# Performance work log

Hardware: AMD Instinct MI355X
Metric: run time of the kernel (lower is better)

## Reference

```python
import jax, jax.numpy as jnp
import numpy as np

NEG = -1000000000.0

def setup_inputs() -> dict:
    key = jax.random.key(0)
    ks = jax.random.split(key, 6)
    B, V, F, H = 8, 4, 256, 768
    video_features = jax.random.normal(ks[0], (B, V, F, H), dtype=jnp.float32)
    video_attention_mask = jax.random.randint(ks[1], (B, V, F), 0, 2) > 0  # True = masked
    s = 1.0 / np.sqrt(H)
    Wqkv = jax.random.normal(ks[2], (3 * H, H), dtype=jnp.float32) * s
    bqkv = jax.random.normal(ks[3], (3 * H,), dtype=jnp.float32) * 0.01
    Wo = jax.random.normal(ks[4], (H, H), dtype=jnp.float32) * s
    bo = jax.random.normal(ks[5], (H,), dtype=jnp.float32) * 0.01
    return {"video_features": video_features, "video_attention_mask": video_attention_mask,
            "Wqkv": Wqkv, "bqkv": bqkv, "Wo": Wo, "bo": bo}

def reference(video_features, video_attention_mask, Wqkv, bqkv, Wo, bo):
    B, V, F, H = video_features.shape
    n_heads = 12
    head_dim = H // n_heads
    S = V * F  # total frames
    x = video_features.reshape(B, S, H)
    mask = video_attention_mask.reshape(B, S)
    # fused QKV projection (torch Linear: x @ W.T + b)
    qkv = x @ Wqkv.T + bqkv                      # [B, S, 3H]
    qkv = qkv.reshape(B, S, n_heads, 3 * head_dim).transpose(0, 2, 1, 3)  # [B, h, S, 3d]
    q, k, v = jnp.split(qkv, 3, axis=-1)         # each [B, h, S, d]
    scores = jnp.einsum('bhqd,bhkd->bhqk', q, k) / np.sqrt(head_dim)
    scores = jnp.where(mask[:, None, None, :], NEG, scores)
    attn = jax.nn.softmax(scores, axis=-1)       # dropout p=0 (eval) -> identity
    out = jnp.einsum('bhqk,bhkd->bhqd', attn, v) # [B, h, S, d]
    out = out.transpose(0, 2, 1, 3).reshape(B, S, H)
    out = out @ Wo.T + bo
    return out.reshape(B, V, F, H)
```

## Files before the change

### kernel.cpp

```cpp
#include <hip/hip_runtime.h>
#include <stdint.h>

typedef unsigned short u16;
typedef unsigned int u32;
typedef __attribute__((ext_vector_type(8))) unsigned short u16x8;
typedef __attribute__((ext_vector_type(4))) unsigned short u16x4;
typedef __attribute__((ext_vector_type(4))) float f32x4;
typedef __attribute__((ext_vector_type(16))) float f32x16;
typedef __attribute__((ext_vector_type(4))) float floatx4;
typedef __attribute__((ext_vector_type(8))) __bf16 bf16x8;


__device__ __forceinline__ u16 f2bf(float f) {
  union { float f; unsigned u; } c; c.f = f;
  unsigned r = c.u + 0x7fffu + ((c.u >> 16) & 1u);
  return (u16)(r >> 16);
}

__device__ __forceinline__ u32 packbf2(float lo, float hi) {
  return (u32)f2bf(lo) | ((u32)f2bf(hi) << 16);
}

__device__ __forceinline__ bf16x8 ld_bf8(const u16* p) {
  return __builtin_bit_cast(bf16x8, *(const u16x8*)p);
}

__device__ __forceinline__ float fexp2(float x) {
#if __has_builtin(__builtin_amdgcn_exp2f)
  return __builtin_amdgcn_exp2f(x);
#else
  float r; asm("v_exp_f32 %0, %1" : "=v"(r) : "v"(x)); return r;
#endif
}

__device__ __forceinline__ void glds16(const void* g, void* l) {
  __builtin_amdgcn_global_load_lds(
      (const __attribute__((address_space(1))) void*)g,
      (__attribute__((address_space(3))) void*)l, 16, 0, 0);
}

__global__ void convert_kernel(const float* __restrict__ x,
                               const float* __restrict__ w1,
                               const float* __restrict__ w2,
                               u16* __restrict__ xb,
                               u16* __restrict__ w1b,
                               u16* __restrict__ w2b) {
  const long NX = 6291456 / 4, NW1 = 1769472 / 4, NW2 = 589824 / 4;
  const long total = NX + NW1 + NW2;
  for (long i = (long)blockIdx.x * 256 + threadIdx.x; i < total;
       i += (long)gridDim.x * 256) {
    const float* src; u16* dst; long j;
    if (i < NX)            { src = x;  dst = xb;  j = i; }
    else if (i < NX + NW1) { src = w1; dst = w1b; j = i - NX; }
    else                   { src = w2; dst = w2b; j = i - NX - NW1; }
    floatx4 v = ((const floatx4*)src)[j];
    u16x4 o;
    o[0] = f2bf(v[0]); o[1] = f2bf(v[1]); o[2] = f2bf(v[2]); o[3] = f2bf(v[3]);
    ((u16x4*)dst)[j] = o;
  }
}

__global__ __launch_bounds__(256, 2)
void qkv_gemm(const u16* __restrict__ A, const u16* __restrict__ W,
              const float* __restrict__ bias,
              u16* __restrict__ qb, u16* __restrict__ kb, u16* __restrict__ vtb) {
  __shared__ __align__(16) u16 lA[2][128 * 64];
  __shared__ __align__(16) u16 lB[2][128 * 64];
  const int tid = threadIdx.x;
  const int lane = tid & 63, wid = tid >> 6;
  const int wm = wid >> 1, wn = wid & 1;
  const int l15 = lane & 15, l4 = lane >> 4;
  const int h7 = l15 & 7;

  const int p = blockIdx.x;
  const int xcd = p & 7, i = p >> 3;
  const int by = xcd * 8 + i / 18;
  const int bx = i % 18;
  const int rowA0 = by * 128, rowB0 = bx * 128;

  const int rlo = lane >> 3;
  const int swz = (lane & 7) ^ rlo;
  const u16* ga = A + (size_t)(rowA0 + wid * 8 + rlo) * 768 + swz * 8;
  const u16* gb = W + (size_t)(rowB0 + wid * 8 + rlo) * 768 + swz * 8;

  f32x4 acc[4][4];
  const f32x4 vz = {0.f, 0.f, 0.f, 0.f};
#pragma unroll
  for (int ii = 0; ii < 4; ++ii)
#pragma unroll
    for (int j = 0; j < 4; ++j) acc[ii][j] = vz;

#define QSTAGE(buf, k0)                                          \
  {                                                              \
    _Pragma("unroll") for (int j = 0; j < 4; ++j) {              \
      glds16(ga + (k0) + j * 32 * 768, lA[buf] + j * 2048 + wid * 512); \
      glds16(gb + (k0) + j * 32 * 768, lB[buf] + j * 2048 + wid * 512); \
    }                                                            \
  }

  QSTAGE(0, 0);

  for (int ks = 0; ks < 12; ++ks) {
    const int cur = ks & 1;
    __builtin_amdgcn_s_barrier();
    if (ks < 11) {
      QSTAGE(cur ^ 1, (ks + 1) * 64);
      asm volatile("s_waitcnt vmcnt(8)" ::: "memory");
    } else {
      asm volatile("s_waitcnt vmcnt(0)" ::: "memory");
    }
    __builtin_amdgcn_s_barrier();
    __builtin_amdgcn_sched_barrier(0);

    bf16x8 af[4][2], bfr[4][2];
#pragma unroll
    for (int mi = 0; mi < 4; ++mi)
#pragma unroll
      for (int kk = 0; kk < 2; ++kk)
        af[mi][kk] = ld_bf8(lA[cur] + (wm * 64 + mi * 16 + l15) * 64 +
                            (((kk * 4 + l4) ^ h7) * 8));
#pragma unroll
    for (int ni = 0; ni < 4; ++ni)
#pragma unroll
      for (int kk = 0; kk < 2; ++kk)
        bfr[ni][kk] = ld_bf8(lB[cur] + (wn * 64 + ni * 16 + l15) * 64 +
                             (((kk * 4 + l4) ^ h7) * 8));
    __builtin_amdgcn_s_setprio(1);
#pragma unroll
    for (int mi = 0; mi < 4; ++mi)
#pragma unroll
      for (int ni = 0; ni < 4; ++ni)
#pragma unroll
        for (int kk = 0; kk < 2; ++kk)
          acc[mi][ni] = __builtin_amdgcn_mfma_f32_16x16x32_bf16(
              af[mi][kk], bfr[ni][kk], acc[mi][ni], 0, 0, 0);
    __builtin_amdgcn_s_setprio(0);
  }
#undef QSTAGE

  const float QSC = 0.125f * 1.44269504088896f;
#pragma unroll
  for (int ni = 0; ni < 4; ++ni) {
    int n = rowB0 + wn * 64 + ni * 16 + l15;
    int h = n / 192;
    int r3 = n - h * 192;
    int t = r3 >> 6, dd = r3 & 63;
    float bn_ = bias[n];
#pragma unroll
    for (int mi = 0; mi < 4; ++mi) {
#pragma unroll
      for (int r = 0; r < 4; ++r) {
        int m = rowA0 + wm * 64 + mi * 16 + l4 * 4 + r;
        int b = m >> 10, s = m & 1023;
        size_t bh = (size_t)(b * 12 + h);
        float v = acc[mi][ni][r] + bn_;
        if (t == 0)
          qb[bh * 65536 + (size_t)s * 64 + dd] = f2bf(v * QSC);
        else if (t == 1)
          kb[bh * 65536 + (size_t)s * 64 + dd] = f2bf(v);
        else
          vtb[bh * 65536 + (size_t)dd * 1024 + s] = f2bf(v);
      }
    }
  }
}

__global__ __launch_bounds__(256, 3)
void attn_kernel(const u16* __restrict__ qb, const u16* __restrict__ kb,
                 const u16* __restrict__ vtb, const void* __restrict__ maskp,
                 u16* __restrict__ x2) {
  const int bh = blockIdx.x, qt = blockIdx.y;
  const int b = bh / 12, h = bh - b * 12;
  const int tid = threadIdx.x;
  const int w = tid >> 6, lane = tid & 63;
  const int l31 = lane & 31, hi = lane >> 5;

  __shared__ float mbias[1024];
  __shared__ int any_big;
  __shared__ __align__(16) u16 plds[4][32][40];
  __shared__ __align__(16) u16 kvs[16384];

  if (tid == 0) any_big = 0;
  __syncthreads();
  {
    const unsigned* mu = (const unsigned*)maskp;
    int loc = 0;
    for (int i = tid; i < 2048; i += 256)
      if (mu[i] > 1u) loc = 1;
    if (loc) atomicOr(&any_big, 1);
  }
  __syncthreads();
  const float CEXP = 23.0831206542234f;
  if (any_big) {
    const unsigned char* mb = (const unsigned char*)maskp;
    for (int i = tid; i < 1024; i += 256)
      mbias[i] = mb[b * 1024 + i] ? -100000.0f : -CEXP;
  } else {
    const int* mi_ = (const int*)maskp;
    for (int i = tid; i < 1024; i += 256)
      mbias[i] = mi_[b * 1024 + i] ? -100000.0f : -CEXP;
  }

  const size_t base = (size_t)bh * 65536;
  const int q0w = qt * 128 + w * 32;

  const int rlo = lane >> 3;
  const int cg = (lane & 7) ^ (rlo & 7);
  const int srow = w * 8 + rlo;
  const u16* kg0 = kb + base + (size_t)srow * 64 + cg * 8;
  const u16* vg0 = vtb + base + (size_t)srow * 1024 + cg * 8;
  u16* kd0 = kvs + w * 512;
  u16* vd0 = kvs + 4096 + w * 512;

  bf16x8 qf[4];
#pragma unroll
  for (int dstep = 0; dstep < 4; ++dstep)
    qf[dstep] = ld_bf8(qb + base + (size_t)(q0w + l31) * 64 + dstep * 16 + hi * 8);

  f32x16 o[2];
#pragma unroll
  for (int dh = 0; dh < 2; ++dh)
#pragma unroll
    for (int r = 0; r < 16; ++r) o[dh][r] = 0.f;
  float ps = 0.f;

  glds16(kg0, kd0);
  glds16(kg0 + 32 * 64, kd0 + 2048);
  glds16(vg0, vd0);
  glds16(vg0 + 32 * 1024, vd0 + 2048);
  __syncthreads();

  for (int kt = 0; kt < 16; ++kt) {
    const int cur = kt & 1;
    if (kt < 15) {
      const int nxt = cur ^ 1;
      glds16(kg0 + (kt + 1) * 4096, kd0 + nxt * 8192);
      glds16(kg0 + (kt + 1) * 4096 + 32 * 64, kd0 + nxt * 8192 + 2048);
      glds16(vg0 + (kt + 1) * 64, vd0 + nxt * 8192);
      glds16(vg0 + (kt + 1) * 64 + 32 * 1024, vd0 + nxt * 8192 + 2048);
    }

    const u16* Kl = kvs + cur * 8192;
    const u16* Vl = kvs + cur * 8192 + 4096;

#pragma unroll
    for (int kk = 0; kk < 2; ++kk) {
      f32x16 s;
#pragma unroll
      for (int r = 0; r < 16; ++r) s[r] = 0.f;
      const int rk = kk * 32 + l31;
      __builtin_amdgcn_s_setprio(1);
#pragma unroll
      for (int dstep = 0; dstep < 4; ++dstep) {
        bf16x8 kf = ld_bf8(Kl + rk * 64 + ((dstep * 2 + hi) ^ (rk & 7)) * 8);
        s = __builtin_amdgcn_mfma_f32_32x32x16_bf16(kf, qf[dstep], s, 0, 0, 0);
      }
      __builtin_amdgcn_s_setprio(0);
#pragma unroll
      for (int g = 0; g < 4; ++g) {
        f32x4 bv = *(const f32x4*)(mbias + kt * 64 + kk * 32 + g * 8 + hi * 4);
        float p0 = fexp2(s[g * 4 + 0] + bv[0]);
        float p1 = fexp2(s[g * 4 + 1] + bv[1]);
        float p2 = fexp2(s[g * 4 + 2] + bv[2]);
        float p3 = fexp2(s[g * 4 + 3] + bv[3]);
        ps += (p0 + p1) + (p2 + p3);
        const int colb = g * 8 + hi * 4;
        *(u32*)&plds[w][l31][colb]     = packbf2(p0, p1);
        *(u32*)&plds[w][l31][colb + 2] = packbf2(p2, p3);
      }

      __builtin_amdgcn_s_setprio(1);
#pragma unroll
      for (int t = 0; t < 2; ++t) {
        bf16x8 pf = ld_bf8(&plds[w][l31][t * 16 + hi * 8]);
#pragma unroll
        for (int dh = 0; dh < 2; ++dh) {
          const int rv = dh * 32 + l31;
          const int gv = kk * 4 + t * 2 + hi;
          bf16x8 vf = ld_bf8(Vl + rv * 64 + (gv ^ (rv & 7)) * 8);
          o[dh] = __builtin_amdgcn_mfma_f32_32x32x16_bf16(vf, pf, o[dh], 0, 0, 0);
        }
      }
      __builtin_amdgcn_s_setprio(0);
    }

    __syncthreads();
  }

  ps += __shfl_xor(ps, 32, 64);
  float inv = 1.0f / ps;

  u16* obuf = kvs + w * 2304;
#pragma unroll
  for (int dh = 0; dh < 2; ++dh)
#pragma unroll
    for (int j = 0; j < 8; ++j) {
      u32 v = packbf2(o[dh][2 * j] * inv, o[dh][2 * j + 1] * inv);
      int col = dh * 32 + 8 * (j >> 1) + 4 * hi + 2 * (j & 1);
      *(u32*)(obuf + l31 * 72 + col) = v;
    }

  {
    int row2 = lane >> 1, ch = lane & 1;
    const u16* srcp = obuf + row2 * 72 + ch * 32;
    u16x8 t0 = *(const u16x8*)(srcp);
    u16x8 t1 = *(const u16x8*)(srcp + 8);
    u16x8 t2 = *(const u16x8*)(srcp + 16);
    u16x8 t3 = *(const u16x8*)(srcp + 24);
    size_t m = (size_t)b * 1024 + qt * 128 + w * 32 + row2;
    u16* dst = x2 + m * 768 + h * 64 + ch * 32;
    *(u16x8*)dst = t0;
    *(u16x8*)(dst + 8) = t1;
    *(u16x8*)(dst + 16) = t2;
    *(u16x8*)(dst + 24) = t3;
  }
}

__global__ __launch_bounds__(256, 2)
void out_gemm(const u16* __restrict__ A, const u16* __restrict__ W,
              const float* __restrict__ bias, float* __restrict__ out) {
  __shared__ __align__(16) u16 lA[2][128 * 64];
  __shared__ __align__(16) u16 lB[2][128 * 64];
  const int tid = threadIdx.x;
  const int lane = tid & 63, wid = tid >> 6;
  const int wm = wid >> 1, wn = wid & 1;
  const int l15 = lane & 15, l4 = lane >> 4;
  const int h7 = l15 & 7;

  const int p = blockIdx.x;
  const int xcd = p & 7, i = p >> 3;
  const int by = xcd * 8 + i / 6;
  const int bx = i % 6;
  const int rowA0 = by * 128, rowB0 = bx * 128;

  const int rlo = lane >> 3;
  const int swz = (lane & 7) ^ rlo;
  const u16* ga = A + (size_t)(rowA0 + wid * 8 + rlo) * 768 + swz * 8;
  const u16* gb = W + (size_t)(rowB0 + wid * 8 + rlo) * 768 + swz * 8;

  f32x4 acc[4][4];
  const f32x4 vz = {0.f, 0.f, 0.f, 0.f};
#pragma unroll
  for (int ii = 0; ii < 4; ++ii)
#pragma unroll
    for (int j = 0; j < 4; ++j) acc[ii][j] = vz;

#define OSTAGE(buf, k0)                                          \
  {                                                              \
    _Pragma("unroll") for (int j = 0; j < 4; ++j) {              \
      glds16(ga + (k0) + j * 32 * 768, lA[buf] + j * 2048 + wid * 512); \
      glds16(gb + (k0) + j * 32 * 768, lB[buf] + j * 2048 + wid * 512); \
    }                                                            \
  }

  OSTAGE(0, 0);

  for (int ks = 0; ks < 12; ++ks) {
    const int cur = ks & 1;
    __builtin_amdgcn_s_barrier();
    if (ks < 11) {
      OSTAGE(cur ^ 1, (ks + 1) * 64);
      asm volatile("s_waitcnt vmcnt(8)" ::: "memory");
    } else {
      asm volatile("s_waitcnt vmcnt(0)" ::: "memory");
    }
    __builtin_amdgcn_s_barrier();
    __builtin_amdgcn_sched_barrier(0);

    bf16x8 af[4][2], bfr[4][2];
#pragma unroll
    for (int mi = 0; mi < 4; ++mi)
#pragma unroll
      for (int kk = 0; kk < 2; ++kk)
        af[mi][kk] = ld_bf8(lA[cur] + (wm * 64 + mi * 16 + l15) * 64 +
                            (((kk * 4 + l4) ^ h7) * 8));
#pragma unroll
    for (int ni = 0; ni < 4; ++ni)
#pragma unroll
      for (int kk = 0; kk < 2; ++kk)
        bfr[ni][kk] = ld_bf8(lB[cur] + (wn * 64 + ni * 16 + l15) * 64 +
                             (((kk * 4 + l4) ^ h7) * 8));
    __builtin_amdgcn_s_setprio(1);
#pragma unroll
    for (int mi = 0; mi < 4; ++mi)
#pragma unroll
      for (int ni = 0; ni < 4; ++ni)
#pragma unroll
        for (int kk = 0; kk < 2; ++kk)
          acc[mi][ni] = __builtin_amdgcn_mfma_f32_16x16x32_bf16(
              af[mi][kk], bfr[ni][kk], acc[mi][ni], 0, 0, 0);
    __builtin_amdgcn_s_setprio(0);
  }
#undef OSTAGE

#pragma unroll
  for (int ni = 0; ni < 4; ++ni) {
    int n = rowB0 + wn * 64 + ni * 16 + l15;
    float bn_ = bias[n];
#pragma unroll
    for (int mi = 0; mi < 4; ++mi)
#pragma unroll
      for (int r = 0; r < 4; ++r) {
        int m = rowA0 + wm * 64 + mi * 16 + l4 * 4 + r;
        out[(size_t)m * 768 + n] = acc[mi][ni][r] + bn_;
      }
  }
}

extern "C" void kernel_launch(void* const* d_in, const int* in_sizes, int n_in,
                              void* d_out, int out_size, void* d_ws, size_t ws_size,
                              hipStream_t stream) {
  const float* x    = (const float*)d_in[0];
  const void*  mask = d_in[1];
  const float* wqkv = (const float*)d_in[2];
  const float* bqkv = (const float*)d_in[3];
  const float* wo   = (const float*)d_in[4];
  const float* bo   = (const float*)d_in[5];
  float* out = (float*)d_out;

  u16* ws = (u16*)d_ws;
  u16* xbf   = ws;
  u16* wqkvb = ws + 6291456;
  u16* wob   = ws + 8060928;
  u16* qbuf  = ws + 8650752;
  u16* kbuf  = ws + 14942208;
  u16* vtbuf = ws + 21233664;
  u16* x2buf = ws + 27525120;

  convert_kernel<<<2048, 256, 0, stream>>>(x, wqkv, wo, xbf, wqkvb, wob);
  qkv_gemm<<<1152, 256, 0, stream>>>(xbf, wqkvb, bqkv, qbuf, kbuf, vtbuf);
  attn_kernel<<<dim3(96, 8), 256, 0, stream>>>(qbuf, kbuf, vtbuf, mask, x2buf);
  out_gemm<<<384, 256, 0, stream>>>(x2buf, wob, bo, out);
}
```

Before: 127.0 us.

## Retile QKV GEMM to 128x192 head-aligned tiles with LDS-staged coalesced epilogue

The QKV projection GEMM now uses 128x192 output tiles, so each tile covers exactly one head's q/k/v columns. It runs a three-stage LDS pipeline with a K step of 32 and a new swizzled layout that packs two rows per 64-element LDS line. The epilogue stages q, k and transposed v through LDS and writes them with 16-byte coalesced stores, replacing the scattered 2-byte global stores (worst for the transposed V). The cost is more accumulator registers per thread (24 f32x4) and more barriers per K step, which could lower occupancy.

```diff
diff --git a/kernel.cpp b/kernel.cpp
--- a/kernel.cpp
+++ b/kernel.cpp
@@ -64,104 +64,158 @@
 void qkv_gemm(const u16* __restrict__ A, const u16* __restrict__ W,
               const float* __restrict__ bias,
               u16* __restrict__ qb, u16* __restrict__ kb, u16* __restrict__ vtb) {
-  __shared__ __align__(16) u16 lA[2][128 * 64];
-  __shared__ __align__(16) u16 lB[2][128 * 64];
+  __shared__ __align__(16) u16 lds[30720];
   const int tid = threadIdx.x;
   const int lane = tid & 63, wid = tid >> 6;
   const int wm = wid >> 1, wn = wid & 1;
   const int l15 = lane & 15, l4 = lane >> 4;
-  const int h7 = l15 & 7;
 
   const int p = blockIdx.x;
   const int xcd = p & 7, i = p >> 3;
-  const int by = xcd * 8 + i / 18;
-  const int bx = i % 18;
-  const int rowA0 = by * 128, rowB0 = bx * 128;
+  const int by = xcd * 8 + i / 12;
+  const int bx = i % 12;
+  const int rowA0 = by * 128, rowB0 = bx * 192;
 
   const int rlo = lane >> 3;
-  const int swz = (lane & 7) ^ rlo;
-  const u16* ga = A + (size_t)(rowA0 + wid * 8 + rlo) * 768 + swz * 8;
-  const u16* gb = W + (size_t)(rowB0 + wid * 8 + rlo) * 768 + swz * 8;
-
-  f32x4 acc[4][4];
+  const u16* gA[2];
+  const u16* gB[3];
+#pragma unroll
+  for (int c = 0; c < 2; ++c) {
+    int mr = wid * 16 + c * 8 + rlo;
+    int sl = (lane & 7) ^ (mr & 7);
+    gA[c] = A + (size_t)(rowA0 + 2 * mr + (sl >> 2)) * 768 + (sl & 3) * 8;
+  }
+#pragma unroll
+  for (int c = 0; c < 3; ++c) {
+    int mr = wid * 24 + c * 8 + rlo;
+    int sl = (lane & 7) ^ (mr & 7);
+    gB[c] = W + (size_t)(rowB0 + 2 * mr + (sl >> 2)) * 768 + (sl & 3) * 8;
+  }
+
+  f32x4 acc[4][6];
   const f32x4 vz = {0.f, 0.f, 0.f, 0.f};
 #pragma unroll
-  for (int ii = 0; ii < 4; ++ii)
-#pragma unroll
-    for (int j = 0; j < 4; ++j) acc[ii][j] = vz;
-
-#define QSTAGE(buf, k0)                                          \
-  {                                                              \
-    _Pragma("unroll") for (int j = 0; j < 4; ++j) {              \
-      glds16(ga + (k0) + j * 32 * 768, lA[buf] + j * 2048 + wid * 512); \
-      glds16(gb + (k0) + j * 32 * 768, lB[buf] + j * 2048 + wid * 512); \
-    }                                                            \
+  for (int mi = 0; mi < 4; ++mi)
+#pragma unroll
+    for (int nj = 0; nj < 6; ++nj) acc[mi][nj] = vz;
+
+#define QSTAGE(kb_, k0_)                                                   \
+  {                                                                        \
+    u16* bA_ = lds + (kb_) * 4096;                                         \
+    u16* bB_ = lds + 12288 + (kb_) * 6144;                                 \
+    _Pragma("unroll") for (int c = 0; c < 2; ++c)                          \
+        glds16(gA[c] + (k0_), bA_ + (wid * 16 + c * 8) * 64);              \
+    _Pragma("unroll") for (int c = 0; c < 3; ++c)                          \
+        glds16(gB[c] + (k0_), bB_ + (wid * 24 + c * 8) * 64);              \
   }
 
   QSTAGE(0, 0);
-
-  for (int ks = 0; ks < 12; ++ks) {
-    const int cur = ks & 1;
+  QSTAGE(1, 32);
+
+  for (int ks = 0; ks < 24; ++ks) {
+    const int cb = ks % 3;
+    const u16* cA = lds + cb * 4096;
+    const u16* cB = lds + 12288 + cb * 6144;
+
     __builtin_amdgcn_s_barrier();
-    if (ks < 11) {
-      QSTAGE(cur ^ 1, (ks + 1) * 64);
-      asm volatile("s_waitcnt vmcnt(8)" ::: "memory");
+    if (ks < 22) {
+      QSTAGE((ks + 2) % 3, (ks + 2) * 32);
+      asm volatile("s_waitcnt vmcnt(10)" ::: "memory");
+    } else if (ks == 22) {
+      asm volatile("s_waitcnt vmcnt(5)" ::: "memory");
     } else {
       asm volatile("s_waitcnt vmcnt(0)" ::: "memory");
     }
     __builtin_amdgcn_s_barrier();
     __builtin_amdgcn_sched_barrier(0);
 
-    bf16x8 af[4][2], bfr[4][2];
+    bf16x8 af[4], bfr[6];
+#pragma unroll
+    for (int mi = 0; mi < 4; ++mi) {
+      int m = wm * 64 + mi * 16 + l15;
+      int mr = m >> 1;
+      int sp = ((m & 1) * 4 + l4) ^ (mr & 7);
+      af[mi] = ld_bf8(cA + mr * 64 + sp * 8);
+    }
+#pragma unroll
+    for (int nj = 0; nj < 6; ++nj) {
+      int n = wn * 96 + nj * 16 + l15;
+      int mr = n >> 1;
+      int sp = ((n & 1) * 4 + l4) ^ (mr & 7);
+      bfr[nj] = ld_bf8(cB + mr * 64 + sp * 8);
+    }
+    __builtin_amdgcn_s_setprio(1);
 #pragma unroll
     for (int mi = 0; mi < 4; ++mi)
 #pragma unroll
-      for (int kk = 0; kk < 2; ++kk)
-        af[mi][kk] = ld_bf8(lA[cur] + (wm * 64 + mi * 16 + l15) * 64 +
-                            (((kk * 4 + l4) ^ h7) * 8));
-#pragma unroll
-    for (int ni = 0; ni < 4; ++ni)
-#pragma unroll
-      for (int kk = 0; kk < 2; ++kk)
-        bfr[ni][kk] = ld_bf8(lB[cur] + (wn * 64 + ni * 16 + l15) * 64 +
-                             (((kk * 4 + l4) ^ h7) * 8));
-    __builtin_amdgcn_s_setprio(1);
-#pragma unroll
-    for (int mi = 0; mi < 4; ++mi)
-#pragma unroll
-      for (int ni = 0; ni < 4; ++ni)
-#pragma unroll
-        for (int kk = 0; kk < 2; ++kk)
-          acc[mi][ni] = __builtin_amdgcn_mfma_f32_16x16x32_bf16(
-              af[mi][kk], bfr[ni][kk], acc[mi][ni], 0, 0, 0);
+      for (int nj = 0; nj < 6; ++nj)
+        acc[mi][nj] = __builtin_amdgcn_mfma_f32_16x16x32_bf16(
+            af[mi], bfr[nj], acc[mi][nj], 0, 0, 0);
     __builtin_amdgcn_s_setprio(0);
   }
 #undef QSTAGE
 
   const float QSC = 0.125f * 1.44269504088896f;
-#pragma unroll
-  for (int ni = 0; ni < 4; ++ni) {
-    int n = rowB0 + wn * 64 + ni * 16 + l15;
-    int h = n / 192;
-    int r3 = n - h * 192;
-    int t = r3 >> 6, dd = r3 & 63;
-    float bn_ = bias[n];
-#pragma unroll
-    for (int mi = 0; mi < 4; ++mi) {
-#pragma unroll
-      for (int r = 0; r < 4; ++r) {
-        int m = rowA0 + wm * 64 + mi * 16 + l4 * 4 + r;
-        int b = m >> 10, s = m & 1023;
-        size_t bh = (size_t)(b * 12 + h);
-        float v = acc[mi][ni][r] + bn_;
-        if (t == 0)
-          qb[bh * 65536 + (size_t)s * 64 + dd] = f2bf(v * QSC);
-        else if (t == 1)
-          kb[bh * 65536 + (size_t)s * 64 + dd] = f2bf(v);
-        else
-          vtb[bh * 65536 + (size_t)dd * 1024 + s] = f2bf(v);
-      }
-    }
+  const int batch = by >> 3, s0 = (by & 7) * 128;
+  const size_t gbase = (size_t)(batch * 12 + bx) * 65536;
+
+  float bias_v[6];
+#pragma unroll
+  for (int nj = 0; nj < 6; ++nj)
+    bias_v[nj] = bias[rowB0 + wn * 96 + nj * 16 + l15];
+
+  __syncthreads();
+
+#pragma unroll
+  for (int nj = 0; nj < 6; ++nj) {
+    int col0 = wn * 96 + nj * 16;
+    int band = col0 >> 6;
+    int dd = (col0 & 63) + l15;
+    float bv = bias_v[nj];
+    if (band < 2) {
+      float sc = (band == 0) ? QSC : 1.0f;
+      u16* reg = lds + band * 9216;
+#pragma unroll
+      for (int mi = 0; mi < 4; ++mi)
+#pragma unroll
+        for (int r = 0; r < 4; ++r) {
+          int m = wm * 64 + mi * 16 + l4 * 4 + r;
+          reg[m * 72 + dd] = f2bf((acc[mi][nj][r] + bv) * sc);
+        }
+    } else {
+      u16* reg = lds + 18432;
+#pragma unroll
+      for (int mi = 0; mi < 4; ++mi)
+#pragma unroll
+        for (int r = 0; r < 4; r += 2) {
+          int m = wm * 64 + mi * 16 + l4 * 4 + r;
+          *(u32*)&reg[dd * 136 + m] =
+              packbf2(acc[mi][nj][r] + bv, acc[mi][nj][r + 1] + bv);
+        }
+    }
+  }
+  __syncthreads();
+
+#pragma unroll
+  for (int j = 0; j < 4; ++j) {
+    int c = tid + j * 256;
+    int m = c >> 3, dd0 = (c & 7) << 3;
+    u16x8 v = *(const u16x8*)&lds[m * 72 + dd0];
+    *(u16x8*)&qb[gbase + (size_t)(s0 + m) * 64 + dd0] = v;
+  }
+#pragma unroll
+  for (int j = 0; j < 4; ++j) {
+    int c = tid + j * 256;
+    int m = c >> 3, dd0 = (c & 7) << 3;
+    u16x8 v = *(const u16x8*)&lds[9216 + m * 72 + dd0];
+    *(u16x8*)&kb[gbase + (size_t)(s0 + m) * 64 + dd0] = v;
+  }
+#pragma unroll
+  for (int j = 0; j < 4; ++j) {
+    int c = tid + j * 256;
+    int dd = c >> 4, m0 = (c & 15) << 3;
+    u16x8 v = *(const u16x8*)&lds[18432 + dd * 136 + m0];
+    *(u16x8*)&vtb[gbase + (size_t)dd * 1024 + s0 + m0] = v;
   }
 }
 
@@ -428,7 +482,7 @@
   u16* x2buf = ws + 27525120;
 
   convert_kernel<<<2048, 256, 0, stream>>>(x, wqkv, wo, xbf, wqkvb, wob);
-  qkv_gemm<<<1152, 256, 0, stream>>>(xbf, wqkvb, bqkv, qbuf, kbuf, vtbuf);
+  qkv_gemm<<<768, 256, 0, stream>>>(xbf, wqkvb, bqkv, qbuf, kbuf, vtbuf);
   attn_kernel<<<dim3(96, 8), 256, 0, stream>>>(qbuf, kbuf, vtbuf, mask, x2buf);
   out_gemm<<<384, 256, 0, stream>>>(x2buf, wob, bo, out);
 }
```

New measurement: 114.5 us. 9.9% less time.
